# Optimization experiments

Measured on AMD Instinct MI355X. Metric: run time of the kernel, lower is better.

## Reference

```python
import jax, jax.numpy as jnp
import numpy as np

NEG_SLOPE = 0.2  # PyG GATConv default negative_slope


def setup_inputs() -> dict:
    key = jax.random.key(0)
    k_x, k_e, k_w, k_as, k_ad = jax.random.split(key, 5)
    B, F, N, D, E, L = 2, 16, 5000, 128, 40000, 3
    x = jax.random.normal(k_x, (B, F, N, D), dtype=jnp.float32)
    edge_index = jax.random.randint(k_e, (B, F, 2, E), 0, N, dtype=jnp.int64)
    Ws = jax.random.normal(k_w, (L, D, D), dtype=jnp.float32) / np.float32(np.sqrt(D))
    att_src = jax.random.normal(k_as, (L, D), dtype=jnp.float32) / np.float32(np.sqrt(D))
    att_dst = jax.random.normal(k_ad, (L, D), dtype=jnp.float32) / np.float32(np.sqrt(D))
    bias = jnp.zeros((L, D), dtype=jnp.float32)
    return {"x": x, "edge_index": edge_index, "Ws": Ws,
            "att_src": att_src, "att_dst": att_dst, "bias": bias}


def _gat_layer(h, src, dst, n, W, a_s, a_d, b):
    # h: [n, D] node features; src/dst: [E_tot] edge endpoints (self-loops included)
    h2 = h @ W                                   # [n, D] transformed features
    s = h2 @ a_s                                 # [n] per-node source score
    d = h2 @ a_d                                 # [n] per-node dest score
    e = jax.nn.leaky_relu(s[src] + d[dst], NEG_SLOPE)   # [E_tot] raw attention
    m = jax.lax.stop_gradient(jax.ops.segment_max(e, dst, num_segments=n))
    ex = jnp.exp(e - m[dst])                     # numerically stable softmax per dst
    denom = jax.ops.segment_sum(ex, dst, num_segments=n)
    alpha = ex / denom[dst]                      # [E_tot] normalized attention
    out = jax.ops.segment_sum(alpha[:, None] * h2[src], dst, num_segments=n) + b
    return jax.nn.relu(out)


def reference(x, edge_index, Ws, att_src, att_dst, bias):
    B, F, N, D = x.shape
    n = B * F * N
    h = x.reshape(n, D)
    # faithful to torch: (BF,2,E).view(2,-1) is a raw row-major reshape
    ei = edge_index.reshape(2, -1)
    loop = jnp.arange(n, dtype=ei.dtype)         # PyG GATConv adds self-loops
    src = jnp.concatenate([ei[0], loop])
    dst = jnp.concatenate([ei[1], loop])
    for l in range(Ws.shape[0]):                 # fixed small layer loop
        h = _gat_layer(h, src, dst, n, Ws[l], att_src[l], att_dst[l], bias[l])
    return h.reshape(B, F, N, D)
```

## Files before the change

### kernel.cpp

```cpp
#include <hip/hip_runtime.h>
#include <math.h>

#define NODES_TOTAL 160000
#define NODES_REAL  5000
#define D 128
#define NEG 0.2f
#define KP 136
#define HL (128 * KP)
#define WT_L (2 * HL)

typedef unsigned short ushort_t;
typedef unsigned int uint_t;
typedef __attribute__((ext_vector_type(8))) __bf16 bf16x8;
typedef __attribute__((ext_vector_type(4))) float f32x4;
union BF8 { bf16x8 v; ushort_t u[8]; };

__device__ __forceinline__ void split2(float x, ushort_t& hi, ushort_t& lo) {
    unsigned u = __float_as_uint(x);
    hi = (ushort_t)(u >> 16);
    float hif = __uint_as_float(u & 0xffff0000u);
    lo = (ushort_t)(__float_as_uint(x - hif) >> 16);
}
__device__ __forceinline__ uint_t encmax(float f) {
    uint_t b = __float_as_uint(f);
    return b ^ ((uint_t)((int)b >> 31) | 0x80000000u);
}
__device__ __forceinline__ float decmax(uint_t u) {
    uint_t b = (u & 0x80000000u) ? (u ^ 0x80000000u) : ~u;
    return __uint_as_float(b);
}

__global__ void zero_kernel(int* counts, uint_t* gmaxu) {
    int i = blockIdx.x * blockDim.x + threadIdx.x;
    if (i < NODES_REAL) counts[i] = 0;
    if (i < 3) gmaxu[i] = 0u;
}

__global__ void rank_kernel(const int* __restrict__ ei, int* __restrict__ counts,
                            ushort_t* __restrict__ rank16, int Eh) {
    int e = blockIdx.x * blockDim.x + threadIdx.x;
    if (e < Eh) {
        int d = ei[Eh + e];
        int r = atomicAdd(&counts[d], 1);
        rank16[e] = (ushort_t)r;
    }
}

__global__ void scan_kernel(const int* __restrict__ counts, int* __restrict__ offs) {
    __shared__ int sd[1024];
    int t = threadIdx.x;
    int pre[5]; int sum = 0;
    #pragma unroll
    for (int u = 0; u < 5; ++u) {
        int idx = t * 5 + u;
        int c = (idx < NODES_REAL) ? counts[idx] : 0;
        pre[u] = sum; sum += c;
    }
    sd[t] = sum;
    __syncthreads();
    int run = sum;
    for (int o = 1; o < 1024; o <<= 1) {
        int v = (t >= o) ? sd[t - o] : 0;
        __syncthreads();
        sd[t] += v;
        __syncthreads();
    }
    int excl = sd[t] - run;
    #pragma unroll
    for (int u = 0; u < 5; ++u) {
        int idx = t * 5 + u;
        if (idx < NODES_REAL) offs[idx] = excl + pre[u];
    }
    if (t == 1023) offs[NODES_REAL] = excl + run;
}

__global__ void scatter_det(const int* __restrict__ ei, const int* __restrict__ offs,
                            const ushort_t* __restrict__ rank16, ushort_t* __restrict__ esrc,
                            int Eh) {
    int e = blockIdx.x * blockDim.x + threadIdx.x;
    if (e < Eh) {
        int s = ei[e];
        int d = ei[Eh + e];
        esrc[offs[d] + (int)rank16[e]] = (ushort_t)s;
    }
}

__global__ void wsplit_kernel(const float* __restrict__ Ws, ushort_t* __restrict__ Wt) {
    int l  = blockIdx.x >> 3;
    int n  = (blockIdx.x & 7) * 16 + (threadIdx.x >> 4);
    int k0 = (threadIdx.x & 15) * 8;
    const float* src = Ws + (size_t)l * D * D;
    union { ushort_t u[8]; uint4 v; } hi, lo;
    #pragma unroll
    for (int j = 0; j < 8; ++j) split2(src[(size_t)(k0 + j) * D + n], hi.u[j], lo.u[j]);
    ushort_t* dhi = Wt + (size_t)l * WT_L + n * KP + k0;
    *(uint4*)dhi = hi.v;
    *(uint4*)(dhi + HL) = lo.v;
}

__global__ __launch_bounds__(256)
void mlp3_kernel(const float* __restrict__ x, const ushort_t* __restrict__ Wt,
                 const float* __restrict__ bs, float* __restrict__ out) {
    __shared__ ushort_t Wl[WT_L];
    __shared__ float scr[4][2][16][132];
    int tid = threadIdx.x;
    int w = tid >> 6, lane = tid & 63, q = lane >> 4, m16 = lane & 15;
    int row0 = NODES_REAL + blockIdx.x * 128 + w * 32;

    float4 xa[2][4][2];
    #pragma unroll
    for (int rt = 0; rt < 2; ++rt) {
        int r = row0 + rt * 16 + m16;
        if (r > NODES_TOTAL - 1) r = NODES_TOTAL - 1;
        #pragma unroll
        for (int kc = 0; kc < 4; ++kc) {
            const float* gp = x + (size_t)r * D + kc * 32 + q * 8;
            xa[rt][kc][0] = *(const float4*)gp;
            xa[rt][kc][1] = *(const float4*)(gp + 4);
        }
    }

    f32x4 acc[2][8];
    #pragma unroll
    for (int l = 0; l < 3; ++l) {
        __syncthreads();
        {
            const uint4* gw = (const uint4*)(Wt + (size_t)l * WT_L);
            uint4* lw = (uint4*)Wl;
            #pragma unroll
            for (int r = 0; r < 17; ++r) lw[r * 256 + tid] = gw[r * 256 + tid];
        }
        __syncthreads();

        #pragma unroll
        for (int rt = 0; rt < 2; ++rt)
            #pragma unroll
            for (int ct = 0; ct < 8; ++ct) acc[rt][ct] = (f32x4){0.f, 0.f, 0.f, 0.f};

        #pragma unroll
        for (int kc = 0; kc < 4; ++kc) {
            BF8 ahi[2], alo[2];
            #pragma unroll
            for (int rt = 0; rt < 2; ++rt) {
                float xv[8];
                if (l == 0) {
                    float4 v0 = xa[rt][kc][0], v1 = xa[rt][kc][1];
                    xv[0]=v0.x; xv[1]=v0.y; xv[2]=v0.z; xv[3]=v0.w;
                    xv[4]=v1.x; xv[5]=v1.y; xv[6]=v1.z; xv[7]=v1.w;
                } else {
                    const float* sp = &scr[w][rt][m16][kc * 32 + q * 8];
                    float4 v0 = *(const float4*)sp, v1 = *(const float4*)(sp + 4);
                    xv[0]=v0.x; xv[1]=v0.y; xv[2]=v0.z; xv[3]=v0.w;
                    xv[4]=v1.x; xv[5]=v1.y; xv[6]=v1.z; xv[7]=v1.w;
                }
                #pragma unroll
                for (int j = 0; j < 8; ++j) split2(xv[j], ahi[rt].u[j], alo[rt].u[j]);
            }
            #pragma unroll
            for (int ct = 0; ct < 8; ++ct) {
                const ushort_t* bp = Wl + (ct * 16 + m16) * KP + kc * 32 + q * 8;
                bf16x8 bhi = *(const bf16x8*)bp;
                bf16x8 blo = *(const bf16x8*)(bp + HL);
                #pragma unroll
                for (int rt = 0; rt < 2; ++rt) {
                    acc[rt][ct] = __builtin_amdgcn_mfma_f32_16x16x32_bf16(ahi[rt].v, bhi, acc[rt][ct], 0, 0, 0);
                    acc[rt][ct] = __builtin_amdgcn_mfma_f32_16x16x32_bf16(ahi[rt].v, blo, acc[rt][ct], 0, 0, 0);
                    acc[rt][ct] = __builtin_amdgcn_mfma_f32_16x16x32_bf16(alo[rt].v, bhi, acc[rt][ct], 0, 0, 0);
                }
            }
        }
        float bv[8];
        #pragma unroll
        for (int ct = 0; ct < 8; ++ct) bv[ct] = bs[l * D + ct * 16 + m16];
        #pragma unroll
        for (int rt = 0; rt < 2; ++rt)
            #pragma unroll
            for (int ct = 0; ct < 8; ++ct)
                #pragma unroll
                for (int reg = 0; reg < 4; ++reg)
                    scr[w][rt][q * 4 + reg][ct * 16 + m16] =
                        fmaxf(acc[rt][ct][reg] + bv[ct], 0.f);
    }
    #pragma unroll
    for (int i = 0; i < 16; ++i) {
        int rowl = i * 2 + (lane >> 5);
        int rt = rowl >> 4, r16 = rowl & 15;
        int grow = row0 + rowl;
        float4 v = *(const float4*)&scr[w][rt][r16][(lane & 31) * 4];
        if (grow < NODES_TOTAL)
            *(float4*)&out[(size_t)grow * D + (lane & 31) * 4] = v;
    }
}

__global__ __launch_bounds__(256)
void gsmall_kernel(const float* __restrict__ hin, const ushort_t* __restrict__ Wlg,
                   const float* __restrict__ a_s, const float* __restrict__ a_d,
                   float* __restrict__ h2, float* __restrict__ sv, float* __restrict__ dv,
                   uint_t* __restrict__ gmaxu) {
    __shared__ ushort_t Wl[WT_L];
    int tid = threadIdx.x;
    {
        const uint4* gw = (const uint4*)Wlg;
        uint4* lw = (uint4*)Wl;
        #pragma unroll
        for (int r = 0; r < 17; ++r) lw[r * 256 + tid] = gw[r * 256 + tid];
    }
    int w = tid >> 6, lane = tid & 63, q = lane >> 4, m16 = lane & 15;
    int row0 = blockIdx.x * 128 + w * 32;
    f32x4 acc[2][8];
    #pragma unroll
    for (int rt = 0; rt < 2; ++rt)
        #pragma unroll
        for (int ct = 0; ct < 8; ++ct) acc[rt][ct] = (f32x4){0.f, 0.f, 0.f, 0.f};
    float4 xa[2][4][2];
    #pragma unroll
    for (int rt = 0; rt < 2; ++rt) {
        int r = row0 + rt * 16 + m16;
        if (r > NODES_REAL - 1) r = NODES_REAL - 1;
        #pragma unroll
        for (int kc = 0; kc < 4; ++kc) {
            const float* gp = hin + (size_t)r * D + kc * 32 + q * 8;
            xa[rt][kc][0] = *(const float4*)gp;
            xa[rt][kc][1] = *(const float4*)(gp + 4);
        }
    }
    __syncthreads();
    #pragma unroll
    for (int kc = 0; kc < 4; ++kc) {
        BF8 ahi[2], alo[2];
        #pragma unroll
        for (int rt = 0; rt < 2; ++rt) {
            float4 v0 = xa[rt][kc][0], v1 = xa[rt][kc][1];
            float xv[8] = {v0.x, v0.y, v0.z, v0.w, v1.x, v1.y, v1.z, v1.w};
            #pragma unroll
            for (int j = 0; j < 8; ++j) split2(xv[j], ahi[rt].u[j], alo[rt].u[j]);
        }
        #pragma unroll
        for (int ct = 0; ct < 8; ++ct) {
            const ushort_t* bp = Wl + (ct * 16 + m16) * KP + kc * 32 + q * 8;
            bf16x8 bhi = *(const bf16x8*)bp;
            bf16x8 blo = *(const bf16x8*)(bp + HL);
            #pragma unroll
            for (int rt = 0; rt < 2; ++rt) {
                acc[rt][ct] = __builtin_amdgcn_mfma_f32_16x16x32_bf16(ahi[rt].v, bhi, acc[rt][ct], 0, 0, 0);
                acc[rt][ct] = __builtin_amdgcn_mfma_f32_16x16x32_bf16(ahi[rt].v, blo, acc[rt][ct], 0, 0, 0);
                acc[rt][ct] = __builtin_amdgcn_mfma_f32_16x16x32_bf16(alo[rt].v, bhi, acc[rt][ct], 0, 0, 0);
            }
        }
    }
    #pragma unroll
    for (int rt = 0; rt < 2; ++rt)
        #pragma unroll
        for (int reg = 0; reg < 4; ++reg) {
            int grow = row0 + rt * 16 + q * 4 + reg;
            if (grow < NODES_REAL) {
                #pragma unroll
                for (int ct = 0; ct < 8; ++ct)
                    h2[(size_t)grow * D + ct * 16 + m16] = acc[rt][ct][reg];
            }
        }
    float asv[8], adv[8];
    #pragma unroll
    for (int ct = 0; ct < 8; ++ct) { asv[ct] = a_s[ct * 16 + m16]; adv[ct] = a_d[ct * 16 + m16]; }
    #pragma unroll
    for (int rt = 0; rt < 2; ++rt)
        #pragma unroll
        for (int reg = 0; reg < 4; ++reg) {
            float ps = 0.f, pd = 0.f;
            #pragma unroll
            for (int ct = 0; ct < 8; ++ct) {
                float v = acc[rt][ct][reg];
                ps += v * asv[ct]; pd += v * adv[ct];
            }
            #pragma unroll
            for (int o = 1; o < 16; o <<= 1) { ps += __shfl_xor(ps, o); pd += __shfl_xor(pd, o); }
            int grow = row0 + rt * 16 + q * 4 + reg;
            if (m16 == 0 && grow < NODES_REAL) {
                sv[grow] = ps; dv[grow] = pd;
                atomicMax(gmaxu, encmax(ps));
            }
        }
}

__global__ __launch_bounds__(256)
void agg_kernel(const float* __restrict__ h2, const float* __restrict__ sv,
                const float* __restrict__ dv, const int* __restrict__ offs,
                const ushort_t* __restrict__ esrc, const float* __restrict__ bias,
                float* __restrict__ out, const uint_t* __restrict__ gmaxu) {
    int w = threadIdx.x >> 6, lane = threadIdx.x & 63;
    int i = blockIdx.x * 4 + w;
    int start = offs[i], end = offs[i + 1];
    float d_i = dv[i];
    float gm = decmax(*gmaxu) + d_i;
    float m = gm > 0.f ? gm : NEG * gm;
    float ax = 0.f, ay = 0.f, exs = 0.f;
    for (int base = start; base < end; base += 64) {
        int cnt = min(64, end - base);
        int srci = (lane < cnt) ? (int)esrc[base + lane] : 0;
        float sc = sv[srci] + d_i;
        sc = sc > 0.f ? sc : NEG * sc;
        float ex = (lane < cnt) ? __expf(sc - m) : 0.f;
        exs += ex;
        if (cnt == 64) {
            #pragma unroll 4
            for (int j = 0; j < 64; ++j) {
                int   src = __shfl(srci, j);
                float e   = __shfl(ex, j);
                float2 hv = *(const float2*)&h2[(size_t)src * D + 2 * lane];
                ax += e * hv.x; ay += e * hv.y;
            }
        } else {
            for (int j = 0; j < cnt; ++j) {
                int   src = __shfl(srci, j);
                float e   = __shfl(ex, j);
                float2 hv = *(const float2*)&h2[(size_t)src * D + 2 * lane];
                ax += e * hv.x; ay += e * hv.y;
            }
        }
    }
    float scf = sv[i] + d_i; scf = scf > 0.f ? scf : NEG * scf;
    float exf = __expf(scf - m);
    float2 hv = *(const float2*)&h2[(size_t)i * D + 2 * lane];
    ax += exf * hv.x; ay += exf * hv.y;
    #pragma unroll
    for (int o = 1; o < 64; o <<= 1) exs += __shfl_xor(exs, o);
    float rd = 1.f / (exs + exf);
    float2 b2 = *(const float2*)&bias[2 * lane];
    float2 o2 = make_float2(fmaxf(ax * rd + b2.x, 0.f), fmaxf(ay * rd + b2.y, 0.f));
    *(float2*)&out[(size_t)i * D + 2 * lane] = o2;
}

extern "C" void kernel_launch(void* const* d_in, const int* in_sizes, int n_in,
                              void* d_out, int out_size, void* d_ws, size_t ws_size,
                              hipStream_t stream) {
    const float* x   = (const float*)d_in[0];
    const int*   ei  = (const int*)d_in[1];
    const float* Ws  = (const float*)d_in[2];
    const float* as_ = (const float*)d_in[3];
    const float* ad_ = (const float*)d_in[4];
    const float* bs  = (const float*)d_in[5];
    float* out = (float*)d_out;
    int Eh = in_sizes[1] / 2;

    char* ws = (char*)d_ws;
    float*    h2     = (float*)ws;
    float*    bufS   = (float*)(ws + 2560000);
    float*    sv     = (float*)(ws + 5120000);
    float*    dv     = (float*)(ws + 5140000);
    int*      counts = (int*)  (ws + 5160000);
    int*      offs   = (int*)  (ws + 5180000);
    ushort_t* rank16 = (ushort_t*)(ws + 5200016);
    ushort_t* esrc   = (ushort_t*)(ws + 7760016);
    ushort_t* Wt     = (ushort_t*)(ws + 10320016);
    uint_t*   gmaxu  = (uint_t*)(ws + 10528912);

    zero_kernel<<<(NODES_REAL + 255) / 256, 256, 0, stream>>>(counts, gmaxu);
    rank_kernel<<<(Eh + 255) / 256, 256, 0, stream>>>(ei, counts, rank16, Eh);
    scan_kernel<<<1, 1024, 0, stream>>>(counts, offs);
    scatter_det<<<(Eh + 255) / 256, 256, 0, stream>>>(ei, offs, rank16, esrc, Eh);
    wsplit_kernel<<<24, 256, 0, stream>>>(Ws, Wt);

    mlp3_kernel<<<(NODES_TOTAL - NODES_REAL + 127) / 128, 256, 0, stream>>>(x, Wt, bs, out);

    for (int l = 0; l < 3; ++l) {
        const float* hin = (l == 0) ? x : bufS;
        float* hout = (l == 2) ? out : bufS;
        gsmall_kernel<<<(NODES_REAL + 127) / 128, 256, 0, stream>>>(
            hin, Wt + (size_t)l * WT_L, as_ + l * D, ad_ + l * D, h2, sv, dv, gmaxu + l);
        agg_kernel<<<(NODES_REAL + 3) / 4, 256, 0, stream>>>(
            h2, sv, dv, offs, esrc, bs + l * D, hout, gmaxu + l);
    }
}
```

Before: 515.1 us.

## Split MLP tile columns across 8 waves and switch split-precision MFMA to fp16

The isolated-node 3-layer MLP kernel now uses 512 threads, with two waves sharing each 32-row group and each wave computing half of the 128 output columns. This halves the accumulator registers per wave and raises the number of resident waves. It adds block-wide barriers around the scratch writes and a cooperative store. Separately, the hi/lo split of operands changes from bf16 truncation to fp16 conversion with fp16 MFMA, which is cheaper to compute and more precise but risks overflow or underflow for large or tiny values.

```diff
diff --git a/kernel.cpp b/kernel.cpp
--- a/kernel.cpp
+++ b/kernel.cpp
@@ -11,15 +11,15 @@
 
 typedef unsigned short ushort_t;
 typedef unsigned int uint_t;
-typedef __attribute__((ext_vector_type(8))) __bf16 bf16x8;
+typedef _Float16 f16;
+typedef __attribute__((ext_vector_type(8))) _Float16 f16x8;
 typedef __attribute__((ext_vector_type(4))) float f32x4;
-union BF8 { bf16x8 v; ushort_t u[8]; };
-
-__device__ __forceinline__ void split2(float x, ushort_t& hi, ushort_t& lo) {
-    unsigned u = __float_as_uint(x);
-    hi = (ushort_t)(u >> 16);
-    float hif = __uint_as_float(u & 0xffff0000u);
-    lo = (ushort_t)(__float_as_uint(x - hif) >> 16);
+union H8 { f16x8 v; f16 h[8]; ushort_t u[8]; };
+union HU { f16 h; ushort_t u; };
+
+__device__ __forceinline__ void split2h(float x, f16& hi, f16& lo) {
+    hi = (f16)x;
+    lo = (f16)(x - (float)hi);
 }
 __device__ __forceinline__ uint_t encmax(float f) {
     uint_t b = __float_as_uint(f);
@@ -92,20 +92,28 @@
     const float* src = Ws + (size_t)l * D * D;
     union { ushort_t u[8]; uint4 v; } hi, lo;
     #pragma unroll
-    for (int j = 0; j < 8; ++j) split2(src[(size_t)(k0 + j) * D + n], hi.u[j], lo.u[j]);
+    for (int j = 0; j < 8; ++j) {
+        HU h, lw;
+        split2h(src[(size_t)(k0 + j) * D + n], h.h, lw.h);
+        hi.u[j] = h.u; lo.u[j] = lw.u;
+    }
     ushort_t* dhi = Wt + (size_t)l * WT_L + n * KP + k0;
     *(uint4*)dhi = hi.v;
     *(uint4*)(dhi + HL) = lo.v;
 }
 
-__global__ __launch_bounds__(256)
+__global__ __launch_bounds__(512, 2)
 void mlp3_kernel(const float* __restrict__ x, const ushort_t* __restrict__ Wt,
                  const float* __restrict__ bs, float* __restrict__ out) {
     __shared__ ushort_t Wl[WT_L];
     __shared__ float scr[4][2][16][132];
     int tid = threadIdx.x;
-    int w = tid >> 6, lane = tid & 63, q = lane >> 4, m16 = lane & 15;
-    int row0 = NODES_REAL + blockIdx.x * 128 + w * 32;
+    int wv = tid >> 6, lane = tid & 63;
+    int rg = wv >> 1, cg = wv & 1;
+    int q = lane >> 4, m16 = lane & 15;
+    int brow0 = NODES_REAL + blockIdx.x * 128;
+    int row0 = brow0 + rg * 32;
+    int cbase = cg * 64;
 
     float4 xa[2][4][2];
     #pragma unroll
@@ -120,7 +128,7 @@
         }
     }
 
-    f32x4 acc[2][8];
+    f32x4 acc[2][4];
     #pragma unroll
     for (int l = 0; l < 3; ++l) {
         __syncthreads();
@@ -128,18 +136,21 @@
             const uint4* gw = (const uint4*)(Wt + (size_t)l * WT_L);
             uint4* lw = (uint4*)Wl;
             #pragma unroll
-            for (int r = 0; r < 17; ++r) lw[r * 256 + tid] = gw[r * 256 + tid];
+            for (int r = 0; r < 9; ++r) {
+                int idx = r * 512 + tid;
+                if (idx < WT_L / 8) lw[idx] = gw[idx];
+            }
         }
         __syncthreads();
 
         #pragma unroll
         for (int rt = 0; rt < 2; ++rt)
             #pragma unroll
-            for (int ct = 0; ct < 8; ++ct) acc[rt][ct] = (f32x4){0.f, 0.f, 0.f, 0.f};
+            for (int ct = 0; ct < 4; ++ct) acc[rt][ct] = (f32x4){0.f, 0.f, 0.f, 0.f};
 
         #pragma unroll
         for (int kc = 0; kc < 4; ++kc) {
-            BF8 ahi[2], alo[2];
+            H8 ahi[2], alo[2];
             #pragma unroll
             for (int rt = 0; rt < 2; ++rt) {
                 float xv[8];
@@ -148,47 +159,49 @@
                     xv[0]=v0.x; xv[1]=v0.y; xv[2]=v0.z; xv[3]=v0.w;
                     xv[4]=v1.x; xv[5]=v1.y; xv[6]=v1.z; xv[7]=v1.w;
                 } else {
-                    const float* sp = &scr[w][rt][m16][kc * 32 + q * 8];
+                    const float* sp = &scr[rg][rt][m16][kc * 32 + q * 8];
                     float4 v0 = *(const float4*)sp, v1 = *(const float4*)(sp + 4);
                     xv[0]=v0.x; xv[1]=v0.y; xv[2]=v0.z; xv[3]=v0.w;
                     xv[4]=v1.x; xv[5]=v1.y; xv[6]=v1.z; xv[7]=v1.w;
                 }
                 #pragma unroll
-                for (int j = 0; j < 8; ++j) split2(xv[j], ahi[rt].u[j], alo[rt].u[j]);
-            }
-            #pragma unroll
-            for (int ct = 0; ct < 8; ++ct) {
-                const ushort_t* bp = Wl + (ct * 16 + m16) * KP + kc * 32 + q * 8;
-                bf16x8 bhi = *(const bf16x8*)bp;
-                bf16x8 blo = *(const bf16x8*)(bp + HL);
+                for (int j = 0; j < 8; ++j) split2h(xv[j], ahi[rt].h[j], alo[rt].h[j]);
+            }
+            #pragma unroll
+            for (int ct = 0; ct < 4; ++ct) {
+                const ushort_t* bp = Wl + (cbase + ct * 16 + m16) * KP + kc * 32 + q * 8;
+                f16x8 bhi = *(const f16x8*)bp;
+                f16x8 blo = *(const f16x8*)(bp + HL);
                 #pragma unroll
                 for (int rt = 0; rt < 2; ++rt) {
-                    acc[rt][ct] = __builtin_amdgcn_mfma_f32_16x16x32_bf16(ahi[rt].v, bhi, acc[rt][ct], 0, 0, 0);
-                    acc[rt][ct] = __builtin_amdgcn_mfma_f32_16x16x32_bf16(ahi[rt].v, blo, acc[rt][ct], 0, 0, 0);
-                    acc[rt][ct] = __builtin_amdgcn_mfma_f32_16x16x32_bf16(alo[rt].v, bhi, acc[rt][ct], 0, 0, 0);
+                    acc[rt][ct] = __builtin_amdgcn_mfma_f32_16x16x32_f16(ahi[rt].v, bhi, acc[rt][ct], 0, 0, 0);
+                    acc[rt][ct] = __builtin_amdgcn_mfma_f32_16x16x32_f16(ahi[rt].v, blo, acc[rt][ct], 0, 0, 0);
+                    acc[rt][ct] = __builtin_amdgcn_mfma_f32_16x16x32_f16(alo[rt].v, bhi, acc[rt][ct], 0, 0, 0);
                 }
             }
         }
-        float bv[8];
-        #pragma unroll
-        for (int ct = 0; ct < 8; ++ct) bv[ct] = bs[l * D + ct * 16 + m16];
+        __syncthreads();
+        float bv[4];
+        #pragma unroll
+        for (int ct = 0; ct < 4; ++ct) bv[ct] = bs[l * D + cbase + ct * 16 + m16];
         #pragma unroll
         for (int rt = 0; rt < 2; ++rt)
             #pragma unroll
-            for (int ct = 0; ct < 8; ++ct)
+            for (int ct = 0; ct < 4; ++ct)
                 #pragma unroll
                 for (int reg = 0; reg < 4; ++reg)
-                    scr[w][rt][q * 4 + reg][ct * 16 + m16] =
+                    scr[rg][rt][q * 4 + reg][cbase + ct * 16 + m16] =
                         fmaxf(acc[rt][ct][reg] + bv[ct], 0.f);
     }
-    #pragma unroll
-    for (int i = 0; i < 16; ++i) {
-        int rowl = i * 2 + (lane >> 5);
-        int rt = rowl >> 4, r16 = rowl & 15;
-        int grow = row0 + rowl;
-        float4 v = *(const float4*)&scr[w][rt][r16][(lane & 31) * 4];
+    __syncthreads();
+    #pragma unroll
+    for (int it = 0; it < 8; ++it) {
+        int flat = it * 512 + tid;
+        int row = flat >> 5, c4 = flat & 31;
+        int grow = brow0 + row;
+        float4 v = *(const float4*)&scr[row >> 5][(row >> 4) & 1][row & 15][c4 * 4];
         if (grow < NODES_TOTAL)
-            *(float4*)&out[(size_t)grow * D + (lane & 31) * 4] = v;
+            *(float4*)&out[(size_t)grow * D + c4 * 4] = v;
     }
 }
 
@@ -227,24 +240,24 @@
     __syncthreads();
     #pragma unroll
     for (int kc = 0; kc < 4; ++kc) {
-        BF8 ahi[2], alo[2];
+        H8 ahi[2], alo[2];
         #pragma unroll
         for (int rt = 0; rt < 2; ++rt) {
             float4 v0 = xa[rt][kc][0], v1 = xa[rt][kc][1];
             float xv[8] = {v0.x, v0.y, v0.z, v0.w, v1.x, v1.y, v1.z, v1.w};
             #pragma unroll
-            for (int j = 0; j < 8; ++j) split2(xv[j], ahi[rt].u[j], alo[rt].u[j]);
+            for (int j = 0; j < 8; ++j) split2h(xv[j], ahi[rt].h[j], alo[rt].h[j]);
         }
         #pragma unroll
         for (int ct = 0; ct < 8; ++ct) {
             const ushort_t* bp = Wl + (ct * 16 + m16) * KP + kc * 32 + q * 8;
-            bf16x8 bhi = *(const bf16x8*)bp;
-            bf16x8 blo = *(const bf16x8*)(bp + HL);
+            f16x8 bhi = *(const f16x8*)bp;
+            f16x8 blo = *(const f16x8*)(bp + HL);
             #pragma unroll
             for (int rt = 0; rt < 2; ++rt) {
-                acc[rt][ct] = __builtin_amdgcn_mfma_f32_16x16x32_bf16(ahi[rt].v, bhi, acc[rt][ct], 0, 0, 0);
-                acc[rt][ct] = __builtin_amdgcn_mfma_f32_16x16x32_bf16(ahi[rt].v, blo, acc[rt][ct], 0, 0, 0);
-                acc[rt][ct] = __builtin_amdgcn_mfma_f32_16x16x32_bf16(alo[rt].v, bhi, acc[rt][ct], 0, 0, 0);
+                acc[rt][ct] = __builtin_amdgcn_mfma_f32_16x16x32_f16(ahi[rt].v, bhi, acc[rt][ct], 0, 0, 0);
+                acc[rt][ct] = __builtin_amdgcn_mfma_f32_16x16x32_f16(ahi[rt].v, blo, acc[rt][ct], 0, 0, 0);
+                acc[rt][ct] = __builtin_amdgcn_mfma_f32_16x16x32_f16(alo[rt].v, bhi, acc[rt][ct], 0, 0, 0);
             }
         }
     }
@@ -360,7 +373,7 @@
     scatter_det<<<(Eh + 255) / 256, 256, 0, stream>>>(ei, offs, rank16, esrc, Eh);
     wsplit_kernel<<<24, 256, 0, stream>>>(Ws, Wt);
 
-    mlp3_kernel<<<(NODES_TOTAL - NODES_REAL + 127) / 128, 256, 0, stream>>>(x, Wt, bs, out);
+    mlp3_kernel<<<(NODES_TOTAL - NODES_REAL + 127) / 128, 512, 0, stream>>>(x, Wt, bs, out);
 
     for (int l = 0; l < 3; ++l) {
         const float* hin = (l == 0) ? x : bufS;
```

Result: no change. 523.4 us (+1.6%).
